# Performance work log

Measured on AMD Instinct MI355X. Metric: run time of the kernel, lower is better.

## Reference

```python
import jax, jax.numpy as jnp
import numpy as np

E = 256; D = 512; A = 5; NS = 2048; NQ = 8192; NWAY = 5
_OTHERS = np.array([[j for j in range(A) if j != i] for i in range(A)])  # [A, A-1] indices of other agents
_ROWS = np.arange(A)[:, None]


def _ln(x, g, b, eps=1e-5):
    m = x.mean(-1, keepdims=True)
    v = ((x - m) ** 2).mean(-1, keepdims=True)
    return (x - m) * jax.lax.rsqrt(v + eps) * g + b


def _mha(x, in_w, in_b, out_w, out_b, h, mask=None):
    # torch nn.MultiheadAttention (batch_first) self-attention. in_w: [3E,E], out_w: [E,E]
    B, S, Em = x.shape
    hd = Em // h
    qkv = x @ in_w.T + in_b
    q, k, v = jnp.split(qkv, 3, axis=-1)
    q = q.reshape(B, S, h, hd).transpose(0, 2, 1, 3) * (1.0 / np.sqrt(hd))
    k = k.reshape(B, S, h, hd).transpose(0, 2, 1, 3)
    v = v.reshape(B, S, h, hd).transpose(0, 2, 1, 3)
    s = jnp.einsum('bhqd,bhkd->bhqk', q, k)
    if mask is not None:
        s = jnp.where(mask, s, jnp.asarray(-1e9, s.dtype))
    a = jax.nn.softmax(s, axis=-1)
    o = jnp.einsum('bhqk,bhkd->bhqd', a, v).transpose(0, 2, 1, 3).reshape(B, S, Em)
    return o @ out_w.T + out_b


def _forward(support_x, support_y, query_x, n_way, fe0_w1, fe0_b1, fe0_g1, fe0_be1, fe0_w2, fe0_b2, fe0_g2, fe0_be2, fe1_w1, fe1_b1, fe1_g, fe1_be, fe1_w2, fe1_b2, fe2_w1, fe2_b1, fe2_w2, fe2_b2, fe2_g, fe2_be, fe3_w1, fe3_b1, fe3_w2, fe3_b2, fe3_g, fe3_be, fe4_w1, fe4_b1, fe4_w2, fe4_b2, fe4_w3, fe4_b3, msg_enc_w, msg_enc_b, agg_in_w, agg_in_b, agg_out_w, agg_out_b, proc_w1, proc_b1, proc_w2, proc_b2, internal_state, proto_in_w, proto_in_b, proto_out_w, proto_out_b, cls_w1, cls_b1, cls_w2, cls_b2, cls_w3, cls_b3, comm_w, f_w1, f_b1, f_w2, f_b2, f_w3, f_b3):
    # --- per-agent-type feature extractors (eval mode: dropout off) ---
    def fe0(x):
        h = jax.nn.relu(_ln(x @ fe0_w1 + fe0_b1, fe0_g1, fe0_be1))
        return jax.nn.relu(_ln(h @ fe0_w2 + fe0_b2, fe0_g2, fe0_be2))
    def fe1(x):
        h = jax.nn.relu(_ln(x @ fe1_w1 + fe1_b1, fe1_g, fe1_be))
        return jnp.tanh(h @ fe1_w2 + fe1_b2)
    def fe2(x):
        h = jax.nn.relu(x @ fe2_w1 + fe2_b1)
        return jax.nn.relu(_ln(h @ fe2_w2 + fe2_b2, fe2_g, fe2_be))
    def fe3(x):
        h = jax.nn.relu(x @ fe3_w1 + fe3_b1)
        return jax.nn.sigmoid(_ln(h @ fe3_w2 + fe3_b2, fe3_g, fe3_be))
    def fe4(x):
        h = jax.nn.relu(x @ fe4_w1 + fe4_b1)
        h = jax.nn.relu(h @ fe4_w2 + fe4_b2)
        return h @ fe4_w3 + fe4_b3
    feats_s = jnp.stack([fe0(support_x), fe1(support_x), fe2(support_x), fe3(support_x), fe4(support_x)])  # [A,NS,E]
    feats_q = jnp.stack([fe0(query_x), fe1(query_x), fe2(query_x), fe3(query_x), fe4(query_x)])            # [A,NQ,E]

    # --- one communication round: generate -> weight -> MHA-aggregate -> MLP-process ---
    agent_state = feats_s.mean(1) + internal_state                                         # [A,E]
    messages = jnp.tanh(jnp.einsum('ae,aef->af', agent_state, msg_enc_w) + msg_enc_b)      # [A,E]
    wgt = jax.nn.softmax(comm_w, axis=-1)                                                  # [A,A]
    msgs = messages[_OTHERS] * wgt[_ROWS, _OTHERS][..., None]                              # [A,A-1,E]
    def agg_one(m, iw, ib, ow, ob):
        return _mha(m[None], iw, ib, ow, ob, 4)[0].mean(0)
    agg = jax.vmap(agg_one)(msgs, agg_in_w, agg_in_b, agg_out_w, agg_out_b)                # [A,E]
    comb = internal_state + agg
    hh = jax.nn.relu(jnp.einsum('ae,aef->af', comb, proc_w1) + proc_b1)
    ck = jnp.einsum('ae,aef->af', hh, proc_w2) + proc_b2                                   # [A,E] communicated knowledge

    # --- class-masked prototype attention (equivalent to per-class MHA) + logits ---
    mask = support_y[:, None] == support_y[None, :]                                        # [NS,NS]
    counts = jax.ops.segment_sum(jnp.ones(support_y.shape, jnp.float32), support_y, num_segments=n_way)
    def head(fs, fq, cki, piw, pib, pw, pb, c1, c1b, c2, c2b, c3, c3b):
        att = _mha((fs + cki[None])[None], piw, pib, pw, pb, 2, mask[None, None])[0]       # [NS,E]
        psum = jax.ops.segment_sum(att, support_y, num_segments=n_way)
        protos = jnp.where(counts[:, None] > 0, psum / jnp.maximum(counts, 1.0)[:, None], 0.0)  # [n_way,E]
        eq = jnp.concatenate([fq, jnp.broadcast_to(cki, fq.shape)], axis=-1)               # [NQ,2E]
        d2 = (fq * fq).sum(-1, keepdims=True) + (protos * protos).sum(-1)[None, :] - 2.0 * (fq @ protos.T)
        dist = jnp.sqrt(jnp.maximum(d2, 1e-12))                                            # cdist
        c = jax.nn.relu(eq @ c1 + c1b)
        c = jax.nn.relu(c @ c2 + c2b)
        conf = c @ c3 + c3b                                                                # [NQ,1]
        return -dist + conf * 0.1
    logits = jax.vmap(head)(feats_s, feats_q, ck, proto_in_w, proto_in_b, proto_out_w, proto_out_b, cls_w1, cls_b1, cls_w2, cls_b2, cls_w3, cls_b3)  # [A,NQ,n_way]

    # --- decision fusion over concatenated per-agent query features ---
    qcat = feats_q.transpose(1, 0, 2).reshape(NQ, A * E)
    fh = jax.nn.relu(qcat @ f_w1 + f_b1)
    fh = jax.nn.relu(fh @ f_w2 + f_b2)
    fused = fh @ f_w3 + f_b3                                                               # [NQ,1]
    return logits, fused


def setup_inputs() -> dict:
    key = jax.random.key(0)
    ks = iter(jax.random.split(key, 80))
    def rn(shape, scale=1.0):
        return (jax.random.normal(next(ks), shape) * scale).astype(jnp.float32)
    def lin(shape, fan):
        return rn(shape, 1.0 / np.sqrt(fan))
    z = lambda s: jnp.zeros(s, jnp.float32)
    o = lambda s: jnp.ones(s, jnp.float32)
    inp = {}
    inp['support_x'] = rn((NS, D))
    inp['support_y'] = jax.random.randint(next(ks), (NS,), 0, NWAY, dtype=jnp.int32)
    inp['query_x'] = rn((NQ, D))
    inp['n_way'] = NWAY
    inp['fe0_w1'] = lin((D, 2 * E), D); inp['fe0_b1'] = z((2 * E,)); inp['fe0_g1'] = o((2 * E,)); inp['fe0_be1'] = z((2 * E,))
    inp['fe0_w2'] = lin((2 * E, E), 2 * E); inp['fe0_b2'] = z((E,)); inp['fe0_g2'] = o((E,)); inp['fe0_be2'] = z((E,))
    inp['fe1_w1'] = lin((D, E), D); inp['fe1_b1'] = z((E,)); inp['fe1_g'] = o((E,)); inp['fe1_be'] = z((E,))
    inp['fe1_w2'] = lin((E, E), E); inp['fe1_b2'] = z((E,))
    inp['fe2_w1'] = lin((D, 3 * E), D); inp['fe2_b1'] = z((3 * E,))
    inp['fe2_w2'] = lin((3 * E, E), 3 * E); inp['fe2_b2'] = z((E,)); inp['fe2_g'] = o((E,)); inp['fe2_be'] = z((E,))
    inp['fe3_w1'] = lin((D, E), D); inp['fe3_b1'] = z((E,))
    inp['fe3_w2'] = lin((E, E), E); inp['fe3_b2'] = z((E,)); inp['fe3_g'] = o((E,)); inp['fe3_be'] = z((E,))
    inp['fe4_w1'] = lin((D, 2 * E), D); inp['fe4_b1'] = z((2 * E,))
    inp['fe4_w2'] = lin((2 * E, E), 2 * E); inp['fe4_b2'] = z((E,))
    inp['fe4_w3'] = lin((E, E), E); inp['fe4_b3'] = z((E,))
    inp['msg_enc_w'] = lin((A, E, E), E); inp['msg_enc_b'] = z((A, E))
    inp['agg_in_w'] = lin((A, 3 * E, E), E); inp['agg_in_b'] = z((A, 3 * E))
    inp['agg_out_w'] = lin((A, E, E), E); inp['agg_out_b'] = z((A, E))
    inp['proc_w1'] = lin((A, E, E), E); inp['proc_b1'] = z((A, E))
    inp['proc_w2'] = lin((A, E, E), E); inp['proc_b2'] = z((A, E))
    inp['internal_state'] = rn((A, E), 0.01)
    inp['proto_in_w'] = lin((A, 3 * E, E), E); inp['proto_in_b'] = z((A, 3 * E))
    inp['proto_out_w'] = lin((A, E, E), E); inp['proto_out_b'] = z((A, E))
    inp['cls_w1'] = lin((A, 2 * E, E), 2 * E); inp['cls_b1'] = z((A, E))
    inp['cls_w2'] = lin((A, E, E // 2), E); inp['cls_b2'] = z((A, E // 2))
    inp['cls_w3'] = lin((A, E // 2, 1), E // 2); inp['cls_b3'] = z((A, 1))
    inp['comm_w'] = (jnp.eye(A) * 0.5 + 0.1).astype(jnp.float32)
    inp['f_w1'] = lin((A * E, E), A * E); inp['f_b1'] = z((E,))
    inp['f_w2'] = lin((E, E // 2), E); inp['f_b2'] = z((E // 2,))
    inp['f_w3'] = lin((E // 2, 1), E // 2); inp['f_b3'] = z((1,))
    return inp


def reference(support_x, support_y, query_x, n_way, fe0_w1, fe0_b1, fe0_g1, fe0_be1, fe0_w2, fe0_b2, fe0_g2, fe0_be2, fe1_w1, fe1_b1, fe1_g, fe1_be, fe1_w2, fe1_b2, fe2_w1, fe2_b1, fe2_w2, fe2_b2, fe2_g, fe2_be, fe3_w1, fe3_b1, fe3_w2, fe3_b2, fe3_g, fe3_be, fe4_w1, fe4_b1, fe4_w2, fe4_b2, fe4_w3, fe4_b3, msg_enc_w, msg_enc_b, agg_in_w, agg_in_b, agg_out_w, agg_out_b, proc_w1, proc_b1, proc_w2, proc_b2, internal_state, proto_in_w, proto_in_b, proto_out_w, proto_out_b, cls_w1, cls_b1, cls_w2, cls_b2, cls_w3, cls_b3, comm_w, f_w1, f_b1, f_w2, f_b2, f_w3, f_b3):
    return _forward(support_x, support_y, query_x, n_way, fe0_w1, fe0_b1, fe0_g1, fe0_be1, fe0_w2, fe0_b2, fe0_g2, fe0_be2, fe1_w1, fe1_b1, fe1_g, fe1_be, fe1_w2, fe1_b2, fe2_w1, fe2_b1, fe2_w2, fe2_b2, fe2_g, fe2_be, fe3_w1, fe3_b1, fe3_w2, fe3_b2, fe3_g, fe3_be, fe4_w1, fe4_b1, fe4_w2, fe4_b2, fe4_w3, fe4_b3, msg_enc_w, msg_enc_b, agg_in_w, agg_in_b, agg_out_w, agg_out_b, proc_w1, proc_b1, proc_w2, proc_b2, internal_state, proto_in_w, proto_in_b, proto_out_w, proto_out_b, cls_w1, cls_b1, cls_w2, cls_b2, cls_w3, cls_b3, comm_w, f_w1, f_b1, f_w2, f_b2, f_w3, f_b3)
```

## Files before the change

### kernel.cpp

```cpp
#include <hip/hip_runtime.h>
#include <hip/hip_bf16.h>

typedef __hip_bfloat16 bf16;
typedef short s8v __attribute__((ext_vector_type(8)));
typedef short s4v __attribute__((ext_vector_type(4)));
typedef float f4v __attribute__((ext_vector_type(4)));

#define A_  5
#define D_  512
#define E_  256
#define NS_ 2048
#define NQ_ 8192
#define NM_ 10240
#define NWAY_ 5
#define QSCALE 0.088388347648318447f
#define FSTR ((size_t)NM_ * E_)

__device__ inline float ldw(const void* p, size_t i, int f32) {
  return f32 ? ((const float*)p)[i] : __bfloat162float(((const bf16*)p)[i]);
}
template<bool DYN>
__device__ inline float ldT(const void* p, size_t i, int f32) {
  if (DYN) return ldw(p, i, f32);
  return ((const float*)p)[i];
}

__device__ inline short f2bf(float v) {
  union { float f; unsigned u; } x; x.f = v;
  unsigned r = x.u + 0x7fffu + ((x.u >> 16) & 1u);
  return (short)(r >> 16);
}
__device__ inline float bf2f(short s) {
  union { unsigned u; float f; } x; x.u = ((unsigned)(unsigned short)s) << 16;
  return x.f;
}

__device__ __forceinline__ void gload16(const void* g, void* l) {
  __builtin_amdgcn_global_load_lds(
      (const __attribute__((address_space(1))) unsigned int*)g,
      (__attribute__((address_space(3))) unsigned int*)l, 16, 0, 0);
}

struct Ptrs { const void* p[64]; int sz[64]; };

__global__ void probe_k(Ptrs P, int* flags) {
  int b = blockIdx.x, lane = threadIdx.x;
  if (b == 1 || b == 3) { if (lane == 0) flags[b] = 0; return; }
  const bf16* t = (const bf16*)P.p[b];
  int n = P.sz[b];
  int K = (n >> 1) < 64 ? (n >> 1) : 64;
  bool big = false, eNZ = false, oNZ = false;
  if (lane < K) {
    float e = __bfloat162float(t[2 * lane]);
    float o = __bfloat162float(t[2 * lane + 1]);
    big = !(fabsf(e) <= 1e3f);
    eNZ = (e != 0.f); oNZ = (o != 0.f);
  }
  unsigned long long bb = __ballot(big), eb = __ballot(eNZ), ob = __ballot(oNZ);
  if (lane == 0) flags[b] = (bb != 0ull || (eb == 0ull && ob != 0ull)) ? 1 : 0;
}

__global__ void classidx_k(const int* __restrict__ y, int* __restrict__ idx,
                           int* __restrict__ cnt, int* __restrict__ cstart) {
  __shared__ int sc[NWAY_];
  int tid = threadIdx.x;
  if (tid < NWAY_) sc[tid] = 0;
  __syncthreads();
  for (int i = tid; i < NS_; i += 256) {
    int c = y[i];
    int pos = atomicAdd(&sc[c], 1);
    idx[c * NS_ + pos] = i;
  }
  __syncthreads();
  if (tid < NWAY_) cnt[tid] = sc[tid];
  if (tid == 0) { int s = 0; for (int q = 0; q < NWAY_; ++q) { cstart[q] = s; s += sc[q]; } }
}

__global__ void xcopy_k(const void* __restrict__ sx, const void* __restrict__ qx,
                        short* __restrict__ XC, const int* __restrict__ flags) {
  size_t i = ((size_t)blockIdx.x * 256 + threadIdx.x) * 4;
  const size_t SN = (size_t)NS_ * 512;
  if (i < SN) {
    int f = flags[0];
    #pragma unroll
    for (int q = 0; q < 4; ++q) XC[i + q] = f2bf(ldw(sx, i + q, f));
  } else {
    int f = flags[2];
    size_t j = i - SN;
    #pragma unroll
    for (int q = 0; q < 4; ++q) XC[i + q] = f2bf(ldw(qx, j + q, f));
  }
}

__global__ void wcat_k(Ptrs P, short* __restrict__ Wcat, float* __restrict__ bcat,
                       const int* __restrict__ flags) {
  int n = blockIdx.x * 256 + threadIdx.x;
  int k = blockIdx.y;
  int iw, ib, nl, Nloc;
  if (n < 512)       { iw = 4;  ib = 5;  nl = n;        Nloc = 512; }
  else if (n < 768)  { iw = 12; ib = 13; nl = n - 512;  Nloc = 256; }
  else if (n < 1536) { iw = 18; ib = 19; nl = n - 768;  Nloc = 768; }
  else if (n < 1792) { iw = 24; ib = 25; nl = n - 1536; Nloc = 256; }
  else               { iw = 30; ib = 31; nl = n - 1792; Nloc = 512; }
  Wcat[(size_t)n * 512 + k] = f2bf(ldw(P.p[iw], (size_t)k * Nloc + nl, flags[iw]));
  if (k == 0) bcat[n] = ldw(P.p[ib], nl, flags[ib]);
}

__global__ void wcls_k(const void* __restrict__ cw1, const void* __restrict__ fw1,
                       short* __restrict__ B2, const int* __restrict__ flags) {
  int n = blockIdx.x, a = blockIdx.y, k = threadIdx.x;
  float v;
  if (n < 256) v = ldw(cw1, ((size_t)a * 512 + k) * 256 + n, flags[51]);
  else v = ldw(fw1, ((size_t)(a * 256 + k)) * 256 + (n - 256), flags[58]);
  B2[((size_t)a * 512 + n) * 256 + k] = f2bf(v);
}

__global__ void wconv_k(Ptrs P, short* __restrict__ W2, const int* __restrict__ flags) {
  const int id = blockIdx.y;
  int src, K, N; size_t off; int tr, batch;
  switch (id) {
    case 0: src = 8;  K = 512; N = 256; off = 0;      tr = 1; batch = 1;  break;
    case 1: src = 16; K = 256; N = 256; off = 131072; tr = 1; batch = 1;  break;
    case 2: src = 20; K = 768; N = 256; off = 196608; tr = 1; batch = 1;  break;
    case 3: src = 26; K = 256; N = 256; off = 393216; tr = 1; batch = 1;  break;
    case 4: src = 32; K = 512; N = 256; off = 458752; tr = 1; batch = 1;  break;
    case 5: src = 34; K = 256; N = 256; off = 589824; tr = 1; batch = 1;  break;
    case 6: src = 53; K = 256; N = 128; off = 655360; tr = 1; batch = A_; break;
    case 7: src = 60; K = 256; N = 128; off = 819200; tr = 1; batch = 1;  break;
    default: src = 47; K = 256; N = 768; off = 851968; tr = 0; batch = A_; break;
  }
  size_t tot = (size_t)batch * K * N;
  size_t e0 = ((size_t)blockIdx.x * 256 + threadIdx.x) * 4;
  if (e0 >= tot) return;
  const void* sp = P.p[src];
  int f = flags[src];
  if (!tr) {
    #pragma unroll
    for (int q = 0; q < 4; ++q) W2[off + e0 + q] = f2bf(ldw(sp, e0 + q, f));
  } else {
    size_t kn = (size_t)K * N;
    #pragma unroll
    for (int q = 0; q < 4; ++q) {
      size_t e = e0 + q;
      int b = (int)(e / kn);
      int r = (int)(e % kn);
      int n = r / K, k = r % K;
      W2[off + e] = f2bf(ldw(sp, ((size_t)b * K + k) * N + n, f));
    }
  }
}

#define LSTR 40
template<int AMODE, int BMODE, bool DYNBIAS, bool TRB, int ACT, bool ACCUM,
         bool KSPLIT = false, bool OUTBF16 = false, bool DOMAP = false>
__global__ __launch_bounds__(256) void gemm_k(
    const void* __restrict__ A, int lda,
    const void* __restrict__ B, int ldb, size_t offB,
    const void* __restrict__ bias, size_t offBias,
    float* __restrict__ C, int ldc,
    int M, int N, int K, float alpha,
    int ia, int ib, int ibias, const int* __restrict__ flags,
    size_t sA, size_t sB, size_t sBias, size_t sC, size_t kstrideA,
    unsigned long long amap)
{
  constexpr bool GDB = (AMODE == 2) && (BMODE == 2) && TRB && !KSPLIT;
  const int fA = (AMODE == 1) ? flags[ia] : 1;
  const int fB = (BMODE == 1) ? flags[ib] : 1;
  const int fBi = DYNBIAS ? flags[ibias] : 1;
  const size_t zA = (size_t)blockIdx.z * sA;
  const size_t zB = offB + (size_t)blockIdx.z * sB;
  const size_t zBias = offBias + (size_t)blockIdx.z * sBias;
  float* Cz = C + (size_t)blockIdx.z * sC;
  bf16* Cz16 = (bf16*)C + (size_t)blockIdx.z * sC;
  const int tid = threadIdx.x;
  const int bm = blockIdx.y * 128, bn = blockIdx.x * 128;
  const int lane = tid & 63, wid = tid >> 6;
  const int lm = lane & 15, quad = lane >> 4;
  const int wy = (wid >> 1) * 64, wx = (wid & 1) * 64;
  f4v acc[4][4];
  #pragma unroll
  for (int i = 0; i < 4; ++i)
    #pragma unroll
    for (int j = 0; j < 4; ++j) acc[i][j] = (f4v)(0.f);

  if constexpr (GDB) {
    __shared__ short smem[4 * 128 * 32];
    const int srow = lane >> 2, scol = (lane & 3) * 8;
    const short* Azs = (const short*)A + zA;
    const short* Bzs = (const short*)B + zB;
    auto stage = [&](int bsel, int k0) {
      short* Asb = smem + bsel * 4096;
      short* Bsb = smem + 8192 + bsel * 4096;
      #pragma unroll
      for (int q = 0; q < 2; ++q) {
        int rb = (wid * 2 + q) * 16;
        gload16(Azs + (size_t)(bm + rb + srow) * lda + k0 + scol, Asb + rb * 32);
        gload16(Bzs + (size_t)(bn + rb + srow) * ldb + k0 + scol, Bsb + rb * 32);
      }
    };
    stage(0, 0);
    __syncthreads();
    int cur = 0;
    for (int k0 = 0; k0 < K; k0 += 32) {
      if (k0 + 32 < K) stage(cur ^ 1, k0 + 32);
      const short* Asb = smem + cur * 4096;
      const short* Bsb = smem + 8192 + cur * 4096;
      s8v af[4], bfr[4];
      #pragma unroll
      for (int mi = 0; mi < 4; ++mi)
        af[mi] = *(const s8v*)&Asb[(wy + mi*16 + lm) * 32 + quad * 8];
      #pragma unroll
      for (int ni = 0; ni < 4; ++ni)
        bfr[ni] = *(const s8v*)&Bsb[(wx + ni*16 + lm) * 32 + quad * 8];
      #pragma unroll
      for (int mi = 0; mi < 4; ++mi)
        #pragma unroll
        for (int ni = 0; ni < 4; ++ni)
          acc[mi][ni] = __builtin_amdgcn_mfma_f32_16x16x32_bf16(af[mi], bfr[ni], acc[mi][ni], 0, 0, 0);
      __syncthreads();
      cur ^= 1;
    }
  } else {
    __shared__ short As[128 * LSTR];
    __shared__ short Bs[128 * LSTR];
    const int am = tid >> 1, ah = (tid & 1) * 16;

    s8v a_s0, a_s1;
    float a_f[16];
    s8v b_s0, b_s1;
    float b_f[16];
    short b_h[16];

    auto loadA = [&](int k0) {
      int kk = k0 + ah;
      size_t base;
      if (KSPLIT) base = zA + (size_t)(kk >> 8) * kstrideA + (size_t)(bm + am) * lda + (kk & 255);
      else base = zA + (size_t)(bm + am) * lda + kk;
      if constexpr (AMODE == 2) {
        const bf16* ap = (const bf16*)A + base;
        a_s0 = *(const s8v*)ap;
        a_s1 = *(const s8v*)(ap + 8);
      } else {
        if (fA) {
          const float4* src = (const float4*)((const float*)A + base);
          #pragma unroll
          for (int q = 0; q < 4; ++q) {
            float4 v = src[q];
            a_f[q*4] = v.x; a_f[q*4+1] = v.y; a_f[q*4+2] = v.z; a_f[q*4+3] = v.w;
          }
        } else {
          #pragma unroll
          for (int q = 0; q < 16; ++q) a_f[q] = ldw(A, base + q, 0);
        }
      }
    };
    auto storeA = [&]() {
      if constexpr (AMODE == 2) {
        *(s8v*)&As[am * LSTR + ah] = a_s0;
        *(s8v*)&As[am * LSTR + ah + 8] = a_s1;
      } else {
        short tmp[16];
        #pragma unroll
        for (int q = 0; q < 16; ++q) tmp[q] = f2bf(a_f[q]);
        s4v* dst = (s4v*)&As[am * LSTR + ah];
        #pragma unroll
        for (int q = 0; q < 4; ++q) dst[q] = *(s4v*)&tmp[q*4];
      }
    };
    auto loadB = [&](int k0) {
      if constexpr (TRB) {
        int n = tid >> 1, h = (tid & 1) * 16;
        size_t base = zB + (size_t)(bn + n) * ldb + k0 + h;
        if constexpr (BMODE == 2) {
          const bf16* bp = (const bf16*)B + base;
          b_s0 = *(const s8v*)bp;
          b_s1 = *(const s8v*)(bp + 8);
        } else {
          if (fB) {
            const float4* src = (const float4*)((const float*)B + base);
            #pragma unroll
            for (int q = 0; q < 4; ++q) {
              float4 v = src[q];
              b_f[q*4] = v.x; b_f[q*4+1] = v.y; b_f[q*4+2] = v.z; b_f[q*4+3] = v.w;
            }
          } else {
            #pragma unroll
            for (int q = 0; q < 16; ++q) b_f[q] = ldw(B, base + q, 0);
          }
        }
      } else {
        int n = tid & 127, kk2 = (tid >> 7) * 16;
        #pragma unroll
        for (int j = 0; j < 16; ++j) {
          size_t bi = zB + (size_t)(k0 + kk2 + j) * ldb + bn + n;
          if constexpr (BMODE == 2) b_h[j] = ((const short*)B)[bi];
          else b_f[j] = ldT<BMODE == 1>(B, bi, fB);
        }
      }
    };
    auto storeB = [&]() {
      if constexpr (TRB) {
        int n = tid >> 1, h = (tid & 1) * 16;
        if constexpr (BMODE == 2) {
          *(s8v*)&Bs[n * LSTR + h] = b_s0;
          *(s8v*)&Bs[n * LSTR + h + 8] = b_s1;
        } else {
          short tmp[16];
          #pragma unroll
          for (int q = 0; q < 16; ++q) tmp[q] = f2bf(b_f[q]);
          s4v* dst = (s4v*)&Bs[n * LSTR + h];
          #pragma unroll
          for (int q = 0; q < 4; ++q) dst[q] = *(s4v*)&tmp[q*4];
        }
      } else {
        int n = tid & 127, kk2 = (tid >> 7) * 16;
        short tmp[16];
        #pragma unroll
        for (int j = 0; j < 16; ++j) tmp[j] = (BMODE == 2) ? b_h[j] : f2bf(b_f[j]);
        s4v* dst = (s4v*)&Bs[n * LSTR + kk2];
        #pragma unroll
        for (int q = 0; q < 4; ++q) dst[q] = *(s4v*)&tmp[q*4];
      }
    };

    loadA(0);
    loadB(0);
    for (int k0 = 0; k0 < K; k0 += 32) {
      storeA();
      storeB();
      __syncthreads();
      if (k0 + 32 < K) { loadA(k0 + 32); loadB(k0 + 32); }
      s8v af[4], bfr[4];
      #pragma unroll
      for (int mi = 0; mi < 4; ++mi)
        af[mi] = *(const s8v*)&As[(wy + mi*16 + lm) * LSTR + quad * 8];
      #pragma unroll
      for (int ni = 0; ni < 4; ++ni)
        bfr[ni] = *(const s8v*)&Bs[(wx + ni*16 + lm) * LSTR + quad * 8];
      #pragma unroll
      for (int mi = 0; mi < 4; ++mi)
        #pragma unroll
        for (int ni = 0; ni < 4; ++ni)
          acc[mi][ni] = __builtin_amdgcn_mfma_f32_16x16x32_bf16(af[mi], bfr[ni], acc[mi][ni], 0, 0, 0);
      __syncthreads();
    }
  }

  const int actc = DOMAP ? (int)((amap >> (((bn + wx) >> 7) * 2)) & 3ULL) : ACT;
  #pragma unroll
  for (int mi = 0; mi < 4; ++mi) {
    #pragma unroll
    for (int r = 0; r < 4; ++r) {
      int row = bm + wy + mi*16 + quad*4 + r;
      #pragma unroll
      for (int ni = 0; ni < 4; ++ni) {
        int col = bn + wx + ni*16 + lm;
        float v = acc[mi][ni][r] * alpha;
        if (ACCUM) v += Cz[(size_t)row * ldc + col];
        if (bias) v += ldT<DYNBIAS>(bias, zBias + col, fBi);
        if (actc == 1) v = fmaxf(v, 0.f);
        else if (actc == 2) v = tanhf(v);
        else if (actc == 3) v = 1.f / (1.f + expf(-v));
        if (OUTBF16) Cz16[(size_t)row * ldc + col] = __float2bfloat16(v);
        else Cz[(size_t)row * ldc + col] = v;
      }
    }
  }
}

template<int AMODE, int BMODE, bool DYNBIAS, bool TRB, int ACT, bool ACCUM,
         bool KSPLIT = false, bool OUTBF16 = false, bool DOMAP = false>
static void gemm(hipStream_t s, const void* A, int lda, const void* B, int ldb, size_t offB,
                 const void* bias, size_t offBias, float* C, int ldc, int M, int N, int K,
                 float alpha, int ia, int ib, int ibias, const int* flags,
                 int batch = 1, size_t sA = 0, size_t sB = 0, size_t sBias = 0, size_t sC = 0,
                 size_t kstrideA = 0, unsigned long long amap = 0) {
  dim3 g(N / 128, M / 128, batch), b(256);
  gemm_k<AMODE, BMODE, DYNBIAS, TRB, ACT, ACCUM, KSPLIT, OUTBF16, DOMAP><<<g, b, 0, s>>>(
      A, lda, B, ldb, offB, bias, offBias, C, ldc, M, N, K, alpha, ia, ib, ibias, flags,
      sA, sB, sBias, sC, kstrideA, amap);
}

template<int ACT, int W>
__global__ __launch_bounds__(256) void lnv_k(const short* __restrict__ X, const void* __restrict__ g,
                                             const void* __restrict__ be, short* __restrict__ Y,
                                             int ldx, int ldy,
                                             int ig, int ibe, const int* __restrict__ flags) {
  const int fG = flags[ig], fBe = flags[ibe];
  const int wid = threadIdx.x >> 6, lane = threadIdx.x & 63;
  const int row = blockIdx.x * 4 + wid;
  constexpr int V = W / 64;
  const short* x = X + (size_t)row * ldx + lane * V;
  float xv[V];
  if constexpr (V == 8) {
    s8v v = *(const s8v*)x;
    #pragma unroll
    for (int q = 0; q < 8; ++q) xv[q] = bf2f(v[q]);
  } else {
    s4v v = *(const s4v*)x;
    #pragma unroll
    for (int q = 0; q < 4; ++q) xv[q] = bf2f(v[q]);
  }
  float s1 = 0.f, s2 = 0.f;
  #pragma unroll
  for (int q = 0; q < V; ++q) { s1 += xv[q]; s2 += xv[q] * xv[q]; }
  #pragma unroll
  for (int o = 32; o > 0; o >>= 1) { s1 += __shfl_xor(s1, o); s2 += __shfl_xor(s2, o); }
  float mean = s1 * (1.f / W);
  float var = fmaxf(s2 * (1.f / W) - mean * mean, 0.f);
  float rstd = rsqrtf(var + 1e-5f);
  short yv[V];
  #pragma unroll
  for (int q = 0; q < V; ++q) {
    int i = lane * V + q;
    float v = (xv[q] - mean) * rstd * ldw(g, i, fG) + ldw(be, i, fBe);
    if (ACT == 1) v = fmaxf(v, 0.f);
    else if (ACT == 3) v = 1.f / (1.f + expf(-v));
    yv[q] = f2bf(v);
  }
  short* y = Y + (size_t)row * ldy + lane * V;
  if constexpr (V == 8) *(s8v*)y = *(s8v*)yv;
  else *(s4v*)y = *(s4v*)yv;
}

__global__ void statepart_k(const short* __restrict__ featsC, float* __restrict__ part) {
  int a = blockIdx.x, g = blockIdx.y, e = threadIdx.x;
  const short* p = featsC + (size_t)a * FSTR + ((size_t)g * 128) * E_ + e;
  float s = 0.f;
  for (int n = 0; n < 128; ++n) s += bf2f(p[(size_t)n * E_]);
  part[((size_t)a * 16 + g) * E_ + e] = s;
}

__global__ void statecomb_k(const float* __restrict__ part, const void* __restrict__ internal,
                            float* __restrict__ state, const int* __restrict__ flags) {
  int a = blockIdx.x, e = threadIdx.x;
  float s = 0.f;
  for (int g = 0; g < 16; ++g) s += part[((size_t)a * 16 + g) * E_ + e];
  state[a * E_ + e] = s * (1.f / NS_) + ldw(internal, (size_t)a * E_ + e, flags[46]);
}

__global__ void mvpart_k(const float* __restrict__ x, const void* __restrict__ W, int iw,
                         float* __restrict__ part, const int* __restrict__ flags) {
  int a = blockIdx.x, g = blockIdx.y, f = threadIdx.x;
  const int fW = flags[iw];
  float s = 0.f;
  size_t wb = (size_t)a * E_ * E_ + f;
  for (int e = g * 32; e < g * 32 + 32; ++e)
    s += x[a * E_ + e] * ldw(W, wb + (size_t)e * E_, fW);
  part[((size_t)a * 8 + g) * E_ + f] = s;
}

template<int ACT>
__global__ void mvcomb_k(const float* __restrict__ part, const void* __restrict__ b, int ibb,
                         float* __restrict__ y, const int* __restrict__ flags) {
  int a = blockIdx.x, f = threadIdx.x;
  float s = 0.f;
  for (int g = 0; g < 8; ++g) s += part[((size_t)a * 8 + g) * E_ + f];
  s += ldw(b, (size_t)a * E_ + f, flags[ibb]);
  if (ACT == 1) s = fmaxf(s, 0.f);
  else if (ACT == 2) s = tanhf(s);
  y[a * E_ + f] = s;
}

__device__ inline float wave_sum64(float v) {
  for (int o = 32; o > 0; o >>= 1) v += __shfl_down(v, o);
  return v;
}

__global__ __launch_bounds__(256) void qkvcomm_k(const float* __restrict__ msg,
                                                 const void* __restrict__ comm_w,
                                                 const void* __restrict__ in_w,
                                                 const void* __restrict__ in_b,
                                                 float* __restrict__ qkvc,
                                                 const int* __restrict__ flags) {
  const int fCW = flags[57], fIW = flags[38], fIB = flags[39];
  int gw = blockIdx.x * 4 + (threadIdx.x >> 6);
  int a = gw / 768, f = gw % 768;
  int lane = threadIdx.x & 63;
  float w[5]; float mx = -1e30f;
  for (int j = 0; j < 5; ++j) { w[j] = ldw(comm_w, a * 5 + j, fCW); mx = fmaxf(mx, w[j]); }
  float sum = 0.f;
  for (int j = 0; j < 5; ++j) { w[j] = __expf(w[j] - mx); sum += w[j]; }
  for (int j = 0; j < 5; ++j) w[j] /= sum;
  int others[4]; { int c = 0; for (int j = 0; j < 5; ++j) if (j != a) others[c++] = j; }
  int e0 = lane * 4;
  float4 wv;
  size_t b = (size_t)a * 768 * E_ + (size_t)f * E_ + e0;
  if (fIW) wv = *(const float4*)((const float*)in_w + b);
  else wv = make_float4(ldw(in_w, b, 0), ldw(in_w, b + 1, 0), ldw(in_w, b + 2, 0), ldw(in_w, b + 3, 0));
  float acc[4];
  #pragma unroll
  for (int t = 0; t < 4; ++t) {
    const float4 mv = *(const float4*)(msg + others[t] * E_ + e0);
    acc[t] = mv.x * wv.x + mv.y * wv.y + mv.z * wv.z + mv.w * wv.w;
  }
  #pragma unroll
  for (int t = 0; t < 4; ++t) acc[t] = wave_sum64(acc[t]);
  if (lane == 0) {
    float bb = ldw(in_b, (size_t)a * 768 + f, fIB);
    #pragma unroll
    for (int t = 0; t < 4; ++t)
      qkvc[((size_t)a * 4 + t) * 768 + f] = acc[t] * w[others[t]] + bb;
  }
}

__global__ __launch_bounds__(256) void attn4_k(const float* __restrict__ qkvc,
                                               float* __restrict__ obar) {
  int a = blockIdx.x, tid = threadIdx.x;
  __shared__ float qkv[4][768];
  __shared__ float attw[4][16];
  for (int i = tid; i < 4 * 768; i += 256) qkv[i / 768][i % 768] = qkvc[(size_t)a * 4 * 768 + i];
  __syncthreads();
  if (tid < 16) {
    int h = tid >> 2, t = tid & 3;
    float sc[4]; float mx = -1e30f;
    for (int t2 = 0; t2 < 4; ++t2) {
      float s = 0.f;
      for (int d = 0; d < 64; ++d) s += qkv[t][h * 64 + d] * qkv[t2][256 + h * 64 + d];
      sc[t2] = s * 0.125f; mx = fmaxf(mx, sc[t2]);
    }
    float ss = 0.f;
    for (int t2 = 0; t2 < 4; ++t2) { sc[t2] = __expf(sc[t2] - mx); ss += sc[t2]; }
    for (int t2 = 0; t2 < 4; ++t2) attw[h][t * 4 + t2] = sc[t2] / ss;
  }
  __syncthreads();
  {
    int e = tid, h = e >> 6;
    float s = 0.f;
    for (int t = 0; t < 4; ++t)
      for (int t2 = 0; t2 < 4; ++t2)
        s += attw[h][t * 4 + t2] * qkv[t2][512 + e];
    obar[a * E_ + e] = s * 0.25f;
  }
}

__global__ __launch_bounds__(256) void combproj_k(const float* __restrict__ obar,
                                                  const void* __restrict__ ow,
                                                  const void* __restrict__ ob,
                                                  const void* __restrict__ internal,
                                                  float* __restrict__ comb,
                                                  const int* __restrict__ flags) {
  const int fOW = flags[40], fOB = flags[41], fIN = flags[46];
  int gw = blockIdx.x * 4 + (threadIdx.x >> 6);
  int a = gw >> 8, f = gw & 255;
  int lane = threadIdx.x & 63;
  int e0 = lane * 4;
  float4 wv;
  size_t b = (size_t)a * E_ * E_ + (size_t)f * E_ + e0;
  if (fOW) wv = *(const float4*)((const float*)ow + b);
  else wv = make_float4(ldw(ow, b, 0), ldw(ow, b + 1, 0), ldw(ow, b + 2, 0), ldw(ow, b + 3, 0));
  const float4 ov = *(const float4*)(obar + a * E_ + e0);
  float s = wave_sum64(ov.x * wv.x + ov.y * wv.y + ov.z * wv.z + ov.w * wv.w);
  if (lane == 0)
    comb[a * E_ + f] = ldw(internal, (size_t)a * E_ + f, fIN) + s + ldw(ob, (size_t)a * E_ + f, fOB);
}

__global__ __launch_bounds__(256) void ckb_k(const float* __restrict__ ck,
                                             const void* __restrict__ in_w,
                                             const void* __restrict__ in_b,
                                             float* __restrict__ ckb,
                                             const int* __restrict__ flags) {
  const int fW = flags[47], fB = flags[48];
  int gw = blockIdx.x * 4 + (threadIdx.x >> 6);
  int a = gw / 768, f = gw % 768;
  int lane = threadIdx.x & 63;
  int e0 = lane * 4;
  float4 wv;
  size_t b = (size_t)a * 768 * E_ + (size_t)f * E_ + e0;
  if (fW) wv = *(const float4*)((const float*)in_w + b);
  else wv = make_float4(ldw(in_w, b, 0), ldw(in_w, b + 1, 0), ldw(in_w, b + 2, 0), ldw(in_w, b + 3, 0));
  const float4 cv = *(const float4*)(ck + a * E_ + e0);
  float s = wave_sum64(cv.x * wv.x + cv.y * wv.y + cv.z * wv.z + cv.w * wv.w);
  if (lane == 0) ckb[(size_t)a * 768 + f] = s + ldw(in_b, (size_t)a * 768 + f, fB);
}

#define LS 136
__device__ inline void stage64x128(const short* __restrict__ qkv, const int* __restrict__ myidx,
                                   int row0, int n, int ho, short* dst) {
  int t = threadIdx.x;
  int r = t >> 2, c0 = (t & 3) * 32;
  int rr = row0 + r;
  s8v v0 = (s8v)(short)0, v1 = v0, v2 = v0, v3 = v0;
  if (rr < n) {
    const s8v* s = (const s8v*)(qkv + (size_t)myidx[rr] * 768 + ho + c0);
    v0 = s[0]; v1 = s[1]; v2 = s[2]; v3 = s[3];
  }
  s8v* d = (s8v*)&dst[r * LS + c0];
  d[0] = v0; d[1] = v1; d[2] = v2; d[3] = v3;
}

__global__ __launch_bounds__(256) void attn_stats_k(
    const short* __restrict__ qkv_all, const int* __restrict__ idx,
    const int* __restrict__ cnt, const int* __restrict__ cstart,
    float* __restrict__ ml)
{
  int c = blockIdx.x, z = blockIdx.z, a = z >> 1, h = z & 1;
  int n = cnt[c];
  int r0 = blockIdx.y * 64;
  if (r0 >= n) return;
  const short* qkv = qkv_all + (size_t)a * NS_ * 768;
  const int* myidx = idx + c * NS_;
  __shared__ short Qs[64 * LS];
  __shared__ short Ks[64 * LS];
  int tid = threadIdx.x, lane = tid & 63, wid = tid >> 6;
  int lm = lane & 15, quad = lane >> 4;
  stage64x128(qkv, myidx, r0, n, h * 128, Qs);
  float m_run = -3e38f, l_run = 0.f;
  for (int j0 = 0; j0 < n; j0 += 64) {
    __syncthreads();
    stage64x128(qkv, myidx, j0, n, 256 + h * 128, Ks);
    __syncthreads();
    f4v acc[4];
    #pragma unroll
    for (int mi = 0; mi < 4; ++mi) acc[mi] = (f4v)(0.f);
    #pragma unroll
    for (int kc = 0; kc < 4; ++kc) {
      s8v qf = *(const s8v*)&Qs[(wid * 16 + lm) * LS + kc * 32 + quad * 8];
      #pragma unroll
      for (int mi = 0; mi < 4; ++mi) {
        s8v kf = *(const s8v*)&Ks[(mi * 16 + lm) * LS + kc * 32 + quad * 8];
        acc[mi] = __builtin_amdgcn_mfma_f32_16x16x32_bf16(kf, qf, acc[mi], 0, 0, 0);
      }
    }
    float sv[16];
    float tm = -3e38f;
    #pragma unroll
    for (int mi = 0; mi < 4; ++mi) {
      #pragma unroll
      for (int r = 0; r < 4; ++r) {
        int kk = j0 + mi * 16 + quad * 4 + r;
        float s = (kk < n) ? acc[mi][r] * QSCALE : -3e38f;
        sv[mi * 4 + r] = s;
        tm = fmaxf(tm, s);
      }
    }
    tm = fmaxf(tm, __shfl_xor(tm, 16));
    tm = fmaxf(tm, __shfl_xor(tm, 32));
    float p = 0.f;
    #pragma unroll
    for (int i = 0; i < 16; ++i) p += __expf(sv[i] - tm);
    p += __shfl_xor(p, 16);
    p += __shfl_xor(p, 32);
    float mn = fmaxf(m_run, tm);
    l_run = l_run * __expf(m_run - mn) + p * __expf(tm - mn);
    m_run = mn;
  }
  int row = r0 + wid * 16 + lm;
  if (quad == 0 && row < n) {
    size_t p = (size_t)z * NS_ + cstart[c] + row;
    ml[p * 2] = m_run; ml[p * 2 + 1] = l_run;
  }
}

__global__ __launch_bounds__(256) void attn_colsum_k(
    const short* __restrict__ qkv_all, const int* __restrict__ idx,
    const int* __restrict__ cnt, const int* __restrict__ cstart,
    const float* __restrict__ ml, float* __restrict__ colsum)
{
  int c = blockIdx.x, z = blockIdx.z, a = z >> 1, h = z & 1;
  int n = cnt[c];
  int j0 = blockIdx.y * 64;
  if (j0 >= n) return;
  const short* qkv = qkv_all + (size_t)a * NS_ * 768;
  const int* myidx = idx + c * NS_;
  __shared__ short Qs[64 * LS];
  __shared__ short Ks[64 * LS];
  __shared__ float Msm[64], Lsm[64];
  int tid = threadIdx.x, lane = tid & 63, wid = tid >> 6;
  int lm = lane & 15, quad = lane >> 4;
  stage64x128(qkv, myidx, j0, n, 256 + h * 128, Ks);
  float ca = 0.f;
  for (int i0 = 0; i0 < n; i0 += 64) {
    __syncthreads();
    stage64x128(qkv, myidx, i0, n, h * 128, Qs);
    if (tid < 64) {
      int gi = i0 + tid;
      if (gi < n) {
        size_t p = (size_t)z * NS_ + cstart[c] + gi;
        Msm[tid] = ml[p * 2]; Lsm[tid] = ml[p * 2 + 1];
      } else { Msm[tid] = 0.f; Lsm[tid] = 1.f; }
    }
    __syncthreads();
    f4v acc[4];
    #pragma unroll
    for (int mi = 0; mi < 4; ++mi) acc[mi] = (f4v)(0.f);
    #pragma unroll
    for (int kc = 0; kc < 4; ++kc) {
      s8v bfr = *(const s8v*)&Ks[(wid * 16 + lm) * LS + kc * 32 + quad * 8];
      #pragma unroll
      for (int mi = 0; mi < 4; ++mi) {
        s8v af = *(const s8v*)&Qs[(mi * 16 + lm) * LS + kc * 32 + quad * 8];
        acc[mi] = __builtin_amdgcn_mfma_f32_16x16x32_bf16(af, bfr, acc[mi], 0, 0, 0);
      }
    }
    #pragma unroll
    for (int mi = 0; mi < 4; ++mi) {
      #pragma unroll
      for (int r = 0; r < 4; ++r) {
        int lrow = mi * 16 + quad * 4 + r;
        int gi = i0 + lrow;
        if (gi < n) {
          float m = Msm[lrow];
          float invl = 1.f / Lsm[lrow];
          ca += __expf(acc[mi][r] * QSCALE - m) * invl;
        }
      }
    }
  }
  ca += __shfl_xor(ca, 16);
  ca += __shfl_xor(ca, 32);
  int col = j0 + wid * 16 + lm;
  if (quad == 0 && col < n)
    colsum[(size_t)z * NS_ + cstart[c] + col] = ca;
}

#define PCH 8
__global__ __launch_bounds__(1024) void proto_reduce_k(
    const short* __restrict__ qkv_all, const int* __restrict__ idx,
    const int* __restrict__ cnt, const int* __restrict__ cstart,
    const float* __restrict__ colsum, float* __restrict__ proto_pre) {
  int c = blockIdx.x, a = blockIdx.y;
  int n = cnt[c];
  int tid = threadIdx.x, lane = tid & 63, wid = tid >> 6;
  int h = lane >> 5;
  int e0 = lane * 4;
  const short* qkv = qkv_all + (size_t)a * NS_ * 768 + 512;
  const float* csum = colsum + (size_t)(a * 2 + h) * NS_ + cstart[c];
  const int* myidx = idx + c * NS_;
  float a0 = 0.f, a1 = 0.f, a2 = 0.f, a3 = 0.f;
  for (int k = wid; k < n; k += 16) {
    float w = csum[k];
    const s4v v = *(const s4v*)(qkv + (size_t)myidx[k] * 768 + e0);
    a0 += w * bf2f(v[0]); a1 += w * bf2f(v[1]);
    a2 += w * bf2f(v[2]); a3 += w * bf2f(v[3]);
  }
  __shared__ float red[16][E_];
  *(float4*)&red[wid][e0] = make_float4(a0, a1, a2, a3);
  __syncthreads();
  if (tid < E_) {
    float s = 0.f;
    #pragma unroll
    for (int wdx = 0; wdx < 16; ++wdx) s += red[wdx][tid];
    proto_pre[((size_t)a * NWAY_ + c) * E_ + tid] = (n > 0) ? s / (float)n : 0.f;
  }
}

__global__ void proto_outproj_k(const float* __restrict__ proto_pre, const void* __restrict__ ow,
                                const void* __restrict__ ob, const int* __restrict__ cnt,
                                float* __restrict__ protos_all, float* __restrict__ pnorm,
                                const int* __restrict__ flags) {
  int c = blockIdx.x, a = blockIdx.y, e = threadIdx.x;
  const int fW = flags[49], fB = flags[50];
  __shared__ float pp[E_];
  __shared__ float r2[E_];
  pp[e] = proto_pre[((size_t)a * NWAY_ + c) * E_ + e];
  __syncthreads();
  size_t wb = (size_t)a * E_ * E_ + (size_t)e * E_;
  float s = 0.f;
  for (int k = 0; k < E_; ++k) s += pp[k] * ldw(ow, wb + k, fW);
  float v = s + ldw(ob, (size_t)a * E_ + e, fB);
  float vm = (cnt[c] > 0) ? v : 0.f;
  protos_all[((size_t)a * NWAY_ + c) * E_ + e] = vm;
  r2[e] = vm * vm;
  __syncthreads();
  for (int o = 128; o > 0; o >>= 1) { if (e < o) r2[e] += r2[e + o]; __syncthreads(); }
  if (e == 0) pnorm[a * NWAY_ + c] = r2[0];
}

__global__ void bias2_k(const float* __restrict__ ck, const void* __restrict__ w1,
                        const void* __restrict__ b1, float* __restrict__ biascat2,
                        const int* __restrict__ flags) {
  const int fW = flags[51], fB = flags[52];
  int a = blockIdx.x, n = threadIdx.x;
  __shared__ float c[E_];
  c[n] = ck[a * E_ + n]; __syncthreads();
  size_t wbase = (size_t)a * 2 * E_ * E_ + (size_t)E_ * E_ + n;
  float s = 0.f;
  for (int k = 0; k < E_; ++k) s += c[k] * ldw(w1, wbase + (size_t)k * E_, fW);
  biascat2[(size_t)a * 512 + n] = s + ldw(b1, (size_t)a * E_ + n, fB);
  biascat2[(size_t)a * 512 + 256 + n] = 0.f;
}

__global__ __launch_bounds__(256) void fcomb2_k(const short* __restrict__ U, const void* __restrict__ b1,
                                                short* __restrict__ fh1, const int* __restrict__ flags) {
  const int fB = flags[59];
  int r = threadIdx.x >> 5;
  int n0 = (threadIdx.x & 31) * 8;
  int i = blockIdx.x * 8 + r;
  float acc[8];
  #pragma unroll
  for (int q = 0; q < 8; ++q) acc[q] = ldw(b1, n0 + q, fB);
  #pragma unroll
  for (int a = 0; a < A_; ++a) {
    s8v v = *(const s8v*)(U + ((size_t)a * NQ_ + i) * 512 + 256 + n0);
    #pragma unroll
    for (int q = 0; q < 8; ++q) acc[q] += bf2f(v[q]);
  }
  short yv[8];
  #pragma unroll
  for (int q = 0; q < 8; ++q) yv[q] = f2bf(fmaxf(acc[q], 0.f));
  *(s8v*)(fh1 + (size_t)i * 256 + n0) = *(s8v*)yv;
}

__global__ __launch_bounds__(256) void logits2_k(const short* __restrict__ fqbase,
                                                 const float* __restrict__ protos_all,
                                                 const float* __restrict__ pnorm,
                                                 const bf16* __restrict__ c2all,
                                                 const void* __restrict__ w3,
                                                 const void* __restrict__ b3,
                                                 float* __restrict__ out,
                                                 const int* __restrict__ flags) {
  const int fW = flags[55], fB = flags[56];
  const int a = blockIdx.y;
  const int i = blockIdx.x * 256 + threadIdx.x;
  __shared__ float ps[NWAY_][E_];
  __shared__ float w3s[128];
  for (int t = threadIdx.x; t < NWAY_ * E_; t += 256)
    ps[t >> 8][t & 255] = protos_all[(size_t)a * NWAY_ * E_ + t];
  if (threadIdx.x < 128) w3s[threadIdx.x] = ldw(w3, (size_t)a * 128 + threadIdx.x, fW);
  __syncthreads();
  const short* fq = fqbase + (size_t)a * FSTR + (size_t)i * E_;
  float qq = 0.f, dt0 = 0.f, dt1 = 0.f, dt2 = 0.f, dt3 = 0.f, dt4 = 0.f;
  for (int e0 = 0; e0 < E_; e0 += 8) {
    s8v v = *(const s8v*)(fq + e0);
    #pragma unroll
    for (int q = 0; q < 8; ++q) {
      float x = bf2f(v[q]); int e = e0 + q;
      qq += x * x;
      dt0 += x * ps[0][e]; dt1 += x * ps[1][e]; dt2 += x * ps[2][e];
      dt3 += x * ps[3][e]; dt4 += x * ps[4][e];
    }
  }
  const short* c2 = (const short*)c2all + ((size_t)a * NQ_ + i) * 128;
  float conf = 0.f;
  for (int e0 = 0; e0 < 128; e0 += 8) {
    s8v v = *(const s8v*)(c2 + e0);
    #pragma unroll
    for (int q = 0; q < 8; ++q) conf += bf2f(v[q]) * w3s[e0 + q];
  }
  conf += ldw(b3, a, fB);
  float dts[5] = { dt0, dt1, dt2, dt3, dt4 };
  float* o = out + ((size_t)a * NQ_ + i) * NWAY_;
  #pragma unroll
  for (int c = 0; c < NWAY_; ++c) {
    float pp = pnorm[a * NWAY_ + c];
    float d2 = fmaxf(qq + pp - 2.f * dts[c], 1e-12f);
    o[c] = -sqrtf(d2) + 0.1f * conf;
  }
}

__global__ __launch_bounds__(256) void fused2_k(const float* __restrict__ h2, const void* __restrict__ w3,
                                                const void* __restrict__ b3, float* __restrict__ out,
                                                const int* __restrict__ flags) {
  const int fW = flags[62], fB = flags[63];
  int i = blockIdx.x * 256 + threadIdx.x;
  __shared__ float ws[128];
  if (threadIdx.x < 128) ws[threadIdx.x] = ldw(w3, threadIdx.x, fW);
  __syncthreads();
  const float* h = h2 + (size_t)i * 128;
  float s = 0.f;
  for (int e = 0; e < 128; e += 4) {
    float4 v = *(const float4*)(h + e);
    s += v.x * ws[e] + v.y * ws[e + 1] + v.z * ws[e + 2] + v.w * ws[e + 3];
  }
  out[i] = s + ldw(b3, 0, fB);
}

extern "C" void kernel_launch(void* const* d_in, const int* in_sizes, int n_in,
                              void* d_out, int out_size, void* d_ws, size_t ws_size,
                              hipStream_t stream) {
  (void)out_size; (void)ws_size;
  #define P(i) ((const void*)d_in[i])
  const int* support_y = (const int*)d_in[1];
  float* out = (float*)d_out;

  int* flags = (int*)d_ws;
  char* base = (char*)d_ws + 256;
  short* featsC = (short*)base;
  char* R = base + (size_t)A_ * FSTR * 2;
  short* t1cat   = (short*)R;
  short* qkv_all = (short*)R;
  short* U       = (short*)(R + (size_t)15728640);
  short* fh1     = (short*)R;
  float* fh2     = (float*)(R + (size_t)8388608);
  char* XCR = R + (size_t)57671680;
  short* XC   = (short*)XCR;
  short* tmp2 = (short*)XCR;
  short* b4   = (short*)(XCR + (size_t)NM_ * 256 * 2);
  short* clsC2_all = (short*)XCR;
  char* S = XCR + (size_t)10485760;
  float* state      = (float*)S;
  float* msg        = state + A_ * E_;
  float* ck         = msg + A_ * E_;
  float* protos_all = ck + A_ * E_;
  float* biascat2   = protos_all + A_ * NWAY_ * E_;
  float* ml         = biascat2 + A_ * 512;
  float* colsum     = ml + (size_t)A_ * 2 * NS_ * 2;
  float* proto_pre  = colsum + (size_t)A_ * 2 * NS_;
  int*   idx        = (int*)(proto_pre + A_ * NWAY_ * E_);
  int*   cnt        = idx + NWAY_ * NS_;
  int*   cstart     = cnt + NWAY_;
  float* statepart  = (float*)(cstart + NWAY_ + 3);
  float* mvp        = statepart + A_ * 16 * E_;
  float* qkvc       = mvp + A_ * 8 * E_;
  float* obar       = qkvc + A_ * 4 * 768;
  float* comb       = obar + A_ * E_;
  float* hh         = comb + A_ * E_;
  float* ckb        = hh + A_ * E_;
  float* ppart      = ckb + A_ * 768;
  float* bcat       = ppart + (size_t)A_ * NWAY_ * PCH * E_;
  short* Wcat       = (short*)(bcat + 2304);
  short* Bcat2      = Wcat + (size_t)2304 * 512;
  short* W2         = Bcat2 + (size_t)A_ * 512 * 256;

  const short* fq_base = featsC + (size_t)NS_ * E_;

  Ptrs ps;
  for (int i = 0; i < 64; ++i) {
    ps.p[i] = (i < n_in) ? d_in[i] : nullptr;
    ps.sz[i] = (i < n_in) ? in_sizes[i] : 0;
  }
  probe_k<<<64, 64, 0, stream>>>(ps, flags);
  classidx_k<<<1, 256, 0, stream>>>(support_y, idx, cnt, cstart);
  xcopy_k<<<(NM_ * 512 / 4) / 256, 256, 0, stream>>>(P(0), P(2), XC, flags);
  wcat_k<<<dim3(9, 512), 256, 0, stream>>>(ps, Wcat, bcat, flags);
  wcls_k<<<dim3(512, A_), 256, 0, stream>>>(P(51), P(58), Bcat2, flags);
  wconv_k<<<dim3(960, 9), 256, 0, stream>>>(ps, W2, flags);

  gemm<2, 2, false, true, 0, false, false, true, true>(
      stream, XC, 512, Wcat, 512, 0, bcat, 0, (float*)t1cat, 2304,
      NM_, 2304, 512, 1.f, -1, -1, -1, flags, 1, 0, 0, 0, 0, 0, 0x555555000ULL);
  lnv_k<1, 512><<<NM_ / 4, 256, 0, stream>>>(t1cat, P(6), P(7), t1cat, 2304, 2304, 6, 7, flags);
  gemm<2, 2, true, true, 0, false, false, true>(stream, t1cat, 2304, W2 + 0, 512, 0, P(9), 0,
                                                (float*)tmp2, 256, NM_, 256, 512, 1.f, -1, -1, 9, flags);
  lnv_k<1, 256><<<NM_ / 4, 256, 0, stream>>>(tmp2, P(10), P(11), featsC, 256, 256, 10, 11, flags);
  lnv_k<1, 256><<<NM_ / 4, 256, 0, stream>>>(t1cat + 512, P(14), P(15), t1cat + 512, 2304, 2304, 14, 15, flags);
  gemm<2, 2, true, true, 2, false, false, true>(stream, t1cat + 512, 2304, W2 + 131072, 256, 0, P(17), 0,
                                                (float*)(featsC + FSTR), 256, NM_, 256, 256, 1.f, -1, -1, 17, flags);
  gemm<2, 2, true, true, 0, false, false, true>(stream, t1cat + 768, 2304, W2 + 196608, 768, 0, P(21), 0,
                                                (float*)tmp2, 256, NM_, 256, 768, 1.f, -1, -1, 21, flags);
  lnv_k<1, 256><<<NM_ / 4, 256, 0, stream>>>(tmp2, P(22), P(23), featsC + 2 * FSTR, 256, 256, 22, 23, flags);
  gemm<2, 2, true, true, 0, false, false, true>(stream, t1cat + 1536, 2304, W2 + 393216, 256, 0, P(27), 0,
                                                (float*)tmp2, 256, NM_, 256, 256, 1.f, -1, -1, 27, flags);
  lnv_k<3, 256><<<NM_ / 4, 256, 0, stream>>>(tmp2, P(28), P(29), featsC + 3 * FSTR, 256, 256, 28, 29, flags);
  gemm<2, 2, true, true, 1, false, false, true>(stream, t1cat + 1792, 2304, W2 + 458752, 512, 0, P(33), 0,
                                                (float*)b4, 256, NM_, 256, 512, 1.f, -1, -1, 33, flags);
  gemm<2, 2, true, true, 0, false, false, true>(stream, b4, 256, W2 + 589824, 256, 0, P(35), 0,
                                                (float*)(featsC + 4 * FSTR), 256, NM_, 256, 256, 1.f, -1, -1, 35, flags);

  statepart_k<<<dim3(A_, 16), 256, 0, stream>>>(featsC, statepart);
  statecomb_k<<<A_, 256, 0, stream>>>(statepart, P(46), state, flags);
  mvpart_k<<<dim3(A_, 8), 256, 0, stream>>>(state, P(36), 36, mvp, flags);
  mvcomb_k<2><<<A_, 256, 0, stream>>>(mvp, P(37), 37, msg, flags);
  qkvcomm_k<<<A_ * 768 / 4, 256, 0, stream>>>(msg, P(57), P(38), P(39), qkvc, flags);
  attn4_k<<<A_, 256, 0, stream>>>(qkvc, obar);
  combproj_k<<<A_ * E_ / 4, 256, 0, stream>>>(obar, P(40), P(41), P(46), comb, flags);
  mvpart_k<<<dim3(A_, 8), 256, 0, stream>>>(comb, P(42), 42, mvp, flags);
  mvcomb_k<1><<<A_, 256, 0, stream>>>(mvp, P(43), 43, hh, flags);
  mvpart_k<<<dim3(A_, 8), 256, 0, stream>>>(hh, P(44), 44, mvp, flags);
  mvcomb_k<0><<<A_, 256, 0, stream>>>(mvp, P(45), 45, ck, flags);

  ckb_k<<<A_ * 768 / 4, 256, 0, stream>>>(ck, P(47), P(48), ckb, flags);
  gemm<2, 2, false, true, 0, false, false, true>(stream, featsC, 256, W2 + 851968, 256, 0, ckb, 0,
                                    (float*)qkv_all, 768, NS_, 768, 256, 1.f, -1, -1, -1, flags,
                                    A_, FSTR, (size_t)768 * 256, (size_t)768, (size_t)NS_ * 768);
  {
    dim3 g(NWAY_, NS_ / 64, A_ * 2);
    attn_stats_k<<<g, 256, 0, stream>>>(qkv_all, idx, cnt, cstart, ml);
    attn_colsum_k<<<g, 256, 0, stream>>>(qkv_all, idx, cnt, cstart, ml, colsum);
  }
  proto_reduce_k<<<dim3(NWAY_, A_), 1024, 0, stream>>>(qkv_all, idx, cnt, cstart, colsum, proto_pre);
  proto_outproj_k<<<dim3(NWAY_, A_), 256, 0, stream>>>(proto_pre, P(49), P(50), cnt, protos_all, ppart, flags);
  bias2_k<<<A_, 256, 0, stream>>>(ck, P(51), P(52), biascat2, flags);

  gemm<2, 2, false, true, 0, false, false, true, true>(
      stream, fq_base, 256, Bcat2, 256, 0, biascat2, 0, (float*)U, 512,
      NQ_, 512, 256, 1.f, -1, -1, -1, flags,
      A_, FSTR, (size_t)512 * 256, (size_t)512, (size_t)NQ_ * 512, 0, 0x5ULL);
  fcomb2_k<<<NQ_ / 8, 256, 0, stream>>>(U, P(59), fh1, flags);

  gemm<2, 2, true, true, 1, false, false, true>(stream, U, 512, W2 + 655360, 256, 0,
                                     P(54), 0, (float*)clsC2_all, 128, NQ_, 128, 256, 1.f, -1, -1, 54, flags,
                                     A_, (size_t)NQ_ * 512, (size_t)128 * 256, (size_t)128, (size_t)NQ_ * 128);
  logits2_k<<<dim3(NQ_ / 256, A_), 256, 0, stream>>>(fq_base, protos_all, ppart,
                                                     (const bf16*)clsC2_all, P(55), P(56), out, flags);

  gemm<2, 2, true, true, 1, false>(stream, fh1, 256, W2 + 819200, 256, 0, P(61), 0, fh2, 128,
                                   NQ_, 128, 256, 1.f, -1, -1, 61, flags);
  fused2_k<<<NQ_ / 256, 256, 0, stream>>>(fh2, P(62), P(63), out + (size_t)A_ * NQ_ * NWAY_, flags);
}
```

Baseline: 803.1 us.

## Batch five per-agent second-layer GEMMs into one grouped kernel launch

```diff
diff --git a/kernel.cpp b/kernel.cpp
--- a/kernel.cpp
+++ b/kernel.cpp
@@ -381,6 +381,86 @@
       sA, sB, sBias, sC, kstrideA, amap);
 }
 
+struct MG5 {
+  const short* A[5]; int K[5];
+  const short* B[5];
+  const void* bias[5]; int ib[5];
+  short* C[5]; int act[5];
+};
+
+__global__ __launch_bounds__(256) void gemm5_k(MG5 P, const int* __restrict__ flags) {
+  const int z = blockIdx.z;
+  const short* A = P.A[z];
+  const short* B = P.B[z];
+  const int K = P.K[z];
+  const int ldb = K;
+  const int actc = P.act[z];
+  const int fBi = flags[P.ib[z]];
+  const void* bias = P.bias[z];
+  short* C = P.C[z];
+  __shared__ short smem[4 * 128 * 32];
+  const int tid = threadIdx.x;
+  const int bm = blockIdx.y * 128, bn = blockIdx.x * 128;
+  const int lane = tid & 63, wid = tid >> 6;
+  const int lm = lane & 15, quad = lane >> 4;
+  const int wy = (wid >> 1) * 64, wx = (wid & 1) * 64;
+  const int srow = lane >> 2, scol = (lane & 3) * 8;
+  f4v acc[4][4];
+  #pragma unroll
+  for (int i = 0; i < 4; ++i)
+    #pragma unroll
+    for (int j = 0; j < 4; ++j) acc[i][j] = (f4v)(0.f);
+
+  auto stage = [&](int bsel, int k0) {
+    short* Asb = smem + bsel * 4096;
+    short* Bsb = smem + 8192 + bsel * 4096;
+    #pragma unroll
+    for (int q = 0; q < 2; ++q) {
+      int rb = (wid * 2 + q) * 16;
+      gload16(A + (size_t)(bm + rb + srow) * 2304 + k0 + scol, Asb + rb * 32);
+      gload16(B + (size_t)(bn + rb + srow) * ldb + k0 + scol, Bsb + rb * 32);
+    }
+  };
+  stage(0, 0);
+  __syncthreads();
+  int cur = 0;
+  for (int k0 = 0; k0 < K; k0 += 32) {
+    if (k0 + 32 < K) stage(cur ^ 1, k0 + 32);
+    const short* Asb = smem + cur * 4096;
+    const short* Bsb = smem + 8192 + cur * 4096;
+    s8v af[4], bfr[4];
+    #pragma unroll
+    for (int mi = 0; mi < 4; ++mi)
+      af[mi] = *(const s8v*)&Asb[(wy + mi*16 + lm) * 32 + quad * 8];
+    #pragma unroll
+    for (int ni = 0; ni < 4; ++ni)
+      bfr[ni] = *(const s8v*)&Bsb[(wx + ni*16 + lm) * 32 + quad * 8];
+    #pragma unroll
+    for (int mi = 0; mi < 4; ++mi)
+      #pragma unroll
+      for (int ni = 0; ni < 4; ++ni)
+        acc[mi][ni] = __builtin_amdgcn_mfma_f32_16x16x32_bf16(af[mi], bfr[ni], acc[mi][ni], 0, 0, 0);
+    __syncthreads();
+    cur ^= 1;
+  }
+
+  #pragma unroll
+  for (int mi = 0; mi < 4; ++mi) {
+    #pragma unroll
+    for (int r = 0; r < 4; ++r) {
+      int row = bm + wy + mi*16 + quad*4 + r;
+      #pragma unroll
+      for (int ni = 0; ni < 4; ++ni) {
+        int col = bn + wx + ni*16 + lm;
+        float v = acc[mi][ni][r] + ldw(bias, col, fBi);
+        if (actc == 1) v = fmaxf(v, 0.f);
+        else if (actc == 2) v = tanhf(v);
+        C[(size_t)row * 256 + col] = f2bf(v);
+      }
+    }
+  }
+}
+
 template<int ACT, int W>
 __global__ __launch_bounds__(256) void lnv_k(const short* __restrict__ X, const void* __restrict__ g,
                                              const void* __restrict__ be, short* __restrict__ Y,
@@ -885,7 +965,6 @@
   float* fh2     = (float*)(R + (size_t)8388608);
   char* XCR = R + (size_t)57671680;
   short* XC   = (short*)XCR;
-  short* tmp2 = (short*)XCR;
   short* b4   = (short*)(XCR + (size_t)NM_ * 256 * 2);
   short* clsC2_all = (short*)XCR;
   char* S = XCR + (size_t)10485760;
@@ -931,20 +1010,21 @@
       stream, XC, 512, Wcat, 512, 0, bcat, 0, (float*)t1cat, 2304,
       NM_, 2304, 512, 1.f, -1, -1, -1, flags, 1, 0, 0, 0, 0, 0, 0x555555000ULL);
   lnv_k<1, 512><<<NM_ / 4, 256, 0, stream>>>(t1cat, P(6), P(7), t1cat, 2304, 2304, 6, 7, flags);
-  gemm<2, 2, true, true, 0, false, false, true>(stream, t1cat, 2304, W2 + 0, 512, 0, P(9), 0,
-                                                (float*)tmp2, 256, NM_, 256, 512, 1.f, -1, -1, 9, flags);
-  lnv_k<1, 256><<<NM_ / 4, 256, 0, stream>>>(tmp2, P(10), P(11), featsC, 256, 256, 10, 11, flags);
   lnv_k<1, 256><<<NM_ / 4, 256, 0, stream>>>(t1cat + 512, P(14), P(15), t1cat + 512, 2304, 2304, 14, 15, flags);
-  gemm<2, 2, true, true, 2, false, false, true>(stream, t1cat + 512, 2304, W2 + 131072, 256, 0, P(17), 0,
-                                                (float*)(featsC + FSTR), 256, NM_, 256, 256, 1.f, -1, -1, 17, flags);
-  gemm<2, 2, true, true, 0, false, false, true>(stream, t1cat + 768, 2304, W2 + 196608, 768, 0, P(21), 0,
-                                                (float*)tmp2, 256, NM_, 256, 768, 1.f, -1, -1, 21, flags);
-  lnv_k<1, 256><<<NM_ / 4, 256, 0, stream>>>(tmp2, P(22), P(23), featsC + 2 * FSTR, 256, 256, 22, 23, flags);
-  gemm<2, 2, true, true, 0, false, false, true>(stream, t1cat + 1536, 2304, W2 + 393216, 256, 0, P(27), 0,
-                                                (float*)tmp2, 256, NM_, 256, 256, 1.f, -1, -1, 27, flags);
-  lnv_k<3, 256><<<NM_ / 4, 256, 0, stream>>>(tmp2, P(28), P(29), featsC + 3 * FSTR, 256, 256, 28, 29, flags);
-  gemm<2, 2, true, true, 1, false, false, true>(stream, t1cat + 1792, 2304, W2 + 458752, 512, 0, P(33), 0,
-                                                (float*)b4, 256, NM_, 256, 512, 1.f, -1, -1, 33, flags);
+
+  {
+    MG5 mg;
+    mg.A[0] = t1cat;        mg.K[0] = 512; mg.B[0] = W2 + 0;      mg.bias[0] = P(9);  mg.ib[0] = 9;  mg.C[0] = featsC;            mg.act[0] = 0;
+    mg.A[1] = t1cat + 512;  mg.K[1] = 256; mg.B[1] = W2 + 131072; mg.bias[1] = P(17); mg.ib[1] = 17; mg.C[1] = featsC + FSTR;     mg.act[1] = 2;
+    mg.A[2] = t1cat + 768;  mg.K[2] = 768; mg.B[2] = W2 + 196608; mg.bias[2] = P(21); mg.ib[2] = 21; mg.C[2] = featsC + 2 * FSTR; mg.act[2] = 0;
+    mg.A[3] = t1cat + 1536; mg.K[3] = 256; mg.B[3] = W2 + 393216; mg.bias[3] = P(27); mg.ib[3] = 27; mg.C[3] = featsC + 3 * FSTR; mg.act[3] = 0;
+    mg.A[4] = t1cat + 1792; mg.K[4] = 512; mg.B[4] = W2 + 458752; mg.bias[4] = P(33); mg.ib[4] = 33; mg.C[4] = b4;                mg.act[4] = 1;
+    dim3 g(2, NM_ / 128, 5), b(256);
+    gemm5_k<<<g, b, 0, stream>>>(mg, flags);
+  }
+  lnv_k<1, 256><<<NM_ / 4, 256, 0, stream>>>(featsC, P(10), P(11), featsC, 256, 256, 10, 11, flags);
+  lnv_k<1, 256><<<NM_ / 4, 256, 0, stream>>>(featsC + 2 * FSTR, P(22), P(23), featsC + 2 * FSTR, 256, 256, 22, 23, flags);
+  lnv_k<3, 256><<<NM_ / 4, 256, 0, stream>>>(featsC + 3 * FSTR, P(28), P(29), featsC + 3 * FSTR, 256, 256, 28, 29, flags);
   gemm<2, 2, true, true, 0, false, false, true>(stream, b4, 256, W2 + 589824, 256, 0, P(35), 0,
                                                 (float*)(featsC + 4 * FSTR), 256, NM_, 256, 256, 1.f, -1, -1, 35, flags);
 
```

After: 735.0 us. 1.09x faster.
